# Kernel tuning notes

Measured on AMD Instinct MI355X. Metric: run time of the kernel, lower is better.

## Reference

```python
import jax, jax.numpy as jnp
import numpy as np

B, H, W = 4, 512, 512   # batch_size and spatial_shape of the SparseConvTensor
N, C = 200000, 256
K, P = 7, 3             # kernel_size, padding (submanifold: K = 2P+1)


def setup_inputs() -> dict:
    key = jax.random.key(0)
    k1, k2, k3, k4 = jax.random.split(key, 4)
    # unique active voxel coordinates via a permutation of the flat grid
    flat = jax.random.permutation(k1, B * H * W)[:N]
    b = (flat // (H * W)).astype(jnp.int32)
    y = ((flat // W) % H).astype(jnp.int32)
    x = (flat % W).astype(jnp.int32)
    indices = jnp.stack([b, y, x], axis=1)  # [N, 3] like spconv (batch, y, x)
    features = jax.random.normal(k2, (N, C), dtype=jnp.float32)
    # per-channel 7x7 depthwise kernels (spconv SubMConv2d(1,1,k) per channel)
    weight = jax.random.normal(k3, (C, K, K), dtype=jnp.float32) * (1.0 / K)
    bias = jax.random.normal(k4, (C,), dtype=jnp.float32) * 0.1
    return {"features": features, "indices": indices, "weight": weight, "bias": bias}


def reference(features, indices, weight, bias):
    """Submanifold depthwise 7x7 conv: outputs only at active sites,
    gathering only active neighbors (inactive sites contribute zero).
    Equivalent to the per-channel SubMConv2d loop, fused across channels."""
    n = features.shape[0]
    b, y, x = indices[:, 0], indices[:, 1], indices[:, 2]
    # dense map from voxel -> row index in features (-1 = inactive); this is the
    # "rulebook" built ONCE and shared by all channels
    idx_map = jnp.full((B, H, W), -1, dtype=jnp.int32)
    idx_map = idx_map.at[b, y, x].set(jnp.arange(n, dtype=jnp.int32))

    out = jnp.zeros_like(features)
    for dy in range(K):          # fixed 7x7 taps: 49-way unroll, vectorized over N, C
        for dx in range(K):
            yy = y + (dy - P)
            xx = x + (dx - P)
            inb = (yy >= 0) & (yy < H) & (xx >= 0) & (xx < W)
            nb = idx_map[b, jnp.clip(yy, 0, H - 1), jnp.clip(xx, 0, W - 1)]
            valid = inb & (nb >= 0)
            f = jnp.where(valid[:, None], features[jnp.maximum(nb, 0)], 0.0)  # [N, C]
            out = out + f * weight[None, :, dy, dx]
    return out + bias[None, :]
```

## Files before the change

### kernel.cpp

```cpp
#include <hip/hip_runtime.h>

#define BB 4
#define HH 512
#define WW 512
#define KK 7
#define PP 3
#define CC 256
#define RH 64
#define RW 32
#define SH (RH + 2 * PP)
#define SW (RW + 2 * PP)
#define NT 1024
#define NWAVE (NT / 64)
#define NREG (BB * (HH / RH) * (WW / RW))

__global__ void smconv_scatter(const int* __restrict__ idx,
                               int* __restrict__ idx_map, int n) {
    int i = blockIdx.x * blockDim.x + threadIdx.x;
    if (i >= n) return;
    int b = idx[i * 3 + 0];
    int y = idx[i * 3 + 1];
    int x = idx[i * 3 + 2];
    idx_map[((size_t)b * HH + y) * WW + x] = i;
}

__global__ void smconv_wt(const float* __restrict__ w, float* __restrict__ w_t) {
    int i = blockIdx.x * blockDim.x + threadIdx.x;
    if (i >= KK * KK * CC) return;
    int tap = i / CC;
    int c = i - tap * CC;
    w_t[i] = w[c * KK * KK + tap];
}

__global__ void __launch_bounds__(NT)
smconv_conv_region(const float* __restrict__ feat,
                   const float* __restrict__ w_t,
                   const float* __restrict__ bias,
                   const int* __restrict__ idx_map,
                   float* __restrict__ out) {
    __shared__ int smap[SH * SW];
    __shared__ unsigned short lst[RH * RW];
    __shared__ int wcnt[NWAVE];
    __shared__ float w_lds[KK * KK * CC];

    const int tid  = threadIdx.x;
    const int wave = tid >> 6;
    const int lane = tid & 63;

    const int r  = (blockIdx.x & 7) * 64 + (blockIdx.x >> 3);
    const int b  = r >> 7;
    const int rm = r & 127;
    const int rx = rm >> 3;
    const int ry = rm & 7;
    const int y0 = ry * RH;
    const int x0 = rx * RW;

    for (int i = tid; i < KK * KK * CC / 4; i += NT)
        ((float4*)w_lds)[i] = ((const float4*)w_t)[i];

    for (int i = tid; i < SH * SW; i += NT) {
        int gy = y0 + i / SW - PP;
        int gx = x0 + i % SW - PP;
        int v = -1;
        if (gy >= 0 && gy < HH && gx >= 0 && gx < WW)
            v = idx_map[((size_t)b * HH + gy) * WW + gx];
        smap[i] = v;
    }
    __syncthreads();

    int total = 0;
    for (int c = 0; c < RH * RW; c += NT) {
        int i = c + tid;
        int iy = i >> 5;
        int ix = i & (RW - 1);
        bool act = smap[(iy + PP) * SW + (ix + PP)] >= 0;
        unsigned long long bal = __ballot(act);
        if (lane == 0) wcnt[wave] = __popcll(bal);
        __syncthreads();
        int off = total;
        for (int w = 0; w < wave; ++w) off += wcnt[w];
        if (act)
            lst[off + __popcll(bal & ((1ull << lane) - 1))] = (unsigned short)i;
        int t2 = total;
        for (int w = 0; w < NWAVE; ++w) t2 += wcnt[w];
        total = t2;
        __syncthreads();
    }

    const int c4 = lane * 4;
    const int dy = lane / KK;
    const int dx = lane % KK;
    const float4 bv = *(const float4*)(bias + c4);

    for (int e = wave; e < total; e += NWAVE) {
        const int pos = lst[e];
        const int iy = pos >> 5;
        const int ix = pos & (RW - 1);

        int nb = -1;
        if (lane < KK * KK)
            nb = smap[(iy + dy) * SW + (ix + dx)];

        const int site = __shfl(nb, PP * KK + PP);
        unsigned long long mask = __ballot(nb >= 0);

        float4 acc = make_float4(0.f, 0.f, 0.f, 0.f);

        while (mask) {
            int t0 = __ffsll((long long)mask) - 1; mask &= mask - 1;
            bool h1 = mask != 0;
            int t1 = h1 ? __ffsll((long long)mask) - 1 : t0;
            if (h1) mask &= mask - 1;
            bool h2 = mask != 0;
            int t2 = h2 ? __ffsll((long long)mask) - 1 : t0;
            if (h2) mask &= mask - 1;
            bool h3 = mask != 0;
            int t3 = h3 ? __ffsll((long long)mask) - 1 : t0;
            if (h3) mask &= mask - 1;

            int n0 = __shfl(nb, t0);
            int n1 = __shfl(nb, t1);
            int n2 = __shfl(nb, t2);
            int n3 = __shfl(nb, t3);

            float4 f0 = *(const float4*)(feat + (size_t)n0 * CC + c4);
            float4 f1 = *(const float4*)(feat + (size_t)n1 * CC + c4);
            float4 f2 = *(const float4*)(feat + (size_t)n2 * CC + c4);
            float4 f3 = *(const float4*)(feat + (size_t)n3 * CC + c4);
            float4 w0 = *(const float4*)(w_lds + t0 * CC + c4);
            float4 w1 = *(const float4*)(w_lds + t1 * CC + c4);
            float4 w2 = *(const float4*)(w_lds + t2 * CC + c4);
            float4 w3 = *(const float4*)(w_lds + t3 * CC + c4);

            acc.x = fmaf(f0.x, w0.x, acc.x);
            acc.y = fmaf(f0.y, w0.y, acc.y);
            acc.z = fmaf(f0.z, w0.z, acc.z);
            acc.w = fmaf(f0.w, w0.w, acc.w);
            if (h1) {
                acc.x = fmaf(f1.x, w1.x, acc.x);
                acc.y = fmaf(f1.y, w1.y, acc.y);
                acc.z = fmaf(f1.z, w1.z, acc.z);
                acc.w = fmaf(f1.w, w1.w, acc.w);
            }
            if (h2) {
                acc.x = fmaf(f2.x, w2.x, acc.x);
                acc.y = fmaf(f2.y, w2.y, acc.y);
                acc.z = fmaf(f2.z, w2.z, acc.z);
                acc.w = fmaf(f2.w, w2.w, acc.w);
            }
            if (h3) {
                acc.x = fmaf(f3.x, w3.x, acc.x);
                acc.y = fmaf(f3.y, w3.y, acc.y);
                acc.z = fmaf(f3.z, w3.z, acc.z);
                acc.w = fmaf(f3.w, w3.w, acc.w);
            }
        }

        float4 o = make_float4(acc.x + bv.x, acc.y + bv.y,
                               acc.z + bv.z, acc.w + bv.w);
        *(float4*)(out + (size_t)site * CC + c4) = o;
    }
}

extern "C" void kernel_launch(void* const* d_in, const int* in_sizes, int n_in,
                              void* d_out, int out_size, void* d_ws, size_t ws_size,
                              hipStream_t stream) {
    const float* feat = (const float*)d_in[0];
    const int*   idx  = (const int*)d_in[1];
    const float* w    = (const float*)d_in[2];
    const float* bias = (const float*)d_in[3];
    float* out = (float*)d_out;

    const int n = in_sizes[0] / CC;

    int*   idx_map = (int*)d_ws;
    float* w_t     = (float*)((char*)d_ws + (size_t)BB * HH * WW * sizeof(int));

    hipMemsetAsync(idx_map, 0xFF, (size_t)BB * HH * WW * sizeof(int), stream);
    smconv_scatter<<<(n + 255) / 256, 256, 0, stream>>>(idx, idx_map, n);
    smconv_wt<<<(KK * KK * CC + 255) / 256, 256, 0, stream>>>(w, w_t);
    smconv_conv_region<<<NREG, NT, 0, stream>>>(feat, w_t, bias, idx_map, out);
}
```

Before: 198.6 us.

## Split channels across two blocks per region with smaller blocks and float2 lanes

Each spatial region is now handled by two 512-thread blocks, each covering 128 channels, so every wave lane processes a float2 rather than a float4. This halves the per-block weight LDS footprint and doubles the block count, aiming for higher occupancy and more concurrent gathers. Lane shuffles for uniform values are replaced with readlane. The cost is that the neighbor map and active list are built twice per region, and each gather row access becomes narrower, 512 bytes per wave.

```diff
diff --git a/kernel.cpp b/kernel.cpp
--- a/kernel.cpp
+++ b/kernel.cpp
@@ -10,9 +10,12 @@
 #define RW 32
 #define SH (RH + 2 * PP)
 #define SW (RW + 2 * PP)
-#define NT 1024
+#define NT 512
 #define NWAVE (NT / 64)
-#define NREG (BB * (HH / RH) * (WW / RW))
+#define NCHUNK 2
+#define CHF 128
+#define NREGN (BB * (HH / RH) * (WW / RW))
+#define NBLK (NREGN * NCHUNK)
 
 __global__ void smconv_scatter(const int* __restrict__ idx,
                                int* __restrict__ idx_map, int n) {
@@ -32,31 +35,36 @@
     w_t[i] = w[c * KK * KK + tap];
 }
 
-__global__ void __launch_bounds__(NT)
-smconv_conv_region(const float* __restrict__ feat,
-                   const float* __restrict__ w_t,
-                   const float* __restrict__ bias,
-                   const int* __restrict__ idx_map,
-                   float* __restrict__ out) {
+__global__ void __launch_bounds__(NT, 8)
+smconv_conv_c2(const float* __restrict__ feat,
+               const float* __restrict__ w_t,
+               const float* __restrict__ bias,
+               const int* __restrict__ idx_map,
+               float* __restrict__ out) {
     __shared__ int smap[SH * SW];
     __shared__ unsigned short lst[RH * RW];
     __shared__ int wcnt[NWAVE];
-    __shared__ float w_lds[KK * KK * CC];
+    __shared__ float w_lds[KK * KK * CHF];
 
     const int tid  = threadIdx.x;
     const int wave = tid >> 6;
     const int lane = tid & 63;
 
-    const int r  = (blockIdx.x & 7) * 64 + (blockIdx.x >> 3);
-    const int b  = r >> 7;
-    const int rm = r & 127;
+    const int Wk    = (blockIdx.x & 7) * (NBLK / 8) + (blockIdx.x >> 3);
+    const int reg   = Wk >> 1;
+    const int chunk = Wk & 1;
+    const int b  = reg >> 7;
+    const int rm = reg & 127;
     const int rx = rm >> 3;
     const int ry = rm & 7;
     const int y0 = ry * RH;
     const int x0 = rx * RW;
 
-    for (int i = tid; i < KK * KK * CC / 4; i += NT)
-        ((float4*)w_lds)[i] = ((const float4*)w_t)[i];
+    for (int i = tid; i < KK * KK * CHF / 4; i += NT) {
+        int t = i >> 5, j = i & 31;
+        ((float4*)w_lds)[i] =
+            ((const float4*)w_t)[t * (CC / 4) + chunk * (CHF / 4) + j];
+    }
 
     for (int i = tid; i < SH * SW; i += NT) {
         int gy = y0 + i / SW - PP;
@@ -69,8 +77,8 @@
     __syncthreads();
 
     int total = 0;
-    for (int c = 0; c < RH * RW; c += NT) {
-        int i = c + tid;
+    for (int c0 = 0; c0 < RH * RW; c0 += NT) {
+        int i = c0 + tid;
         int iy = i >> 5;
         int ix = i & (RW - 1);
         bool act = smap[(iy + PP) * SW + (ix + PP)] >= 0;
@@ -87,10 +95,13 @@
         __syncthreads();
     }
 
-    const int c4 = lane * 4;
     const int dy = lane / KK;
     const int dx = lane % KK;
-    const float4 bv = *(const float4*)(bias + c4);
+    const float2* feat2 = (const float2*)feat;
+    const float2* wlds2 = (const float2*)w_lds;
+    float2* out2 = (float2*)out;
+    const int co = chunk * (CHF / 2) + lane;
+    const float2 bv = ((const float2*)bias)[co];
 
     for (int e = wave; e < total; e += NWAVE) {
         const int pos = lst[e];
@@ -101,64 +112,53 @@
         if (lane < KK * KK)
             nb = smap[(iy + dy) * SW + (ix + dx)];
 
-        const int site = __shfl(nb, PP * KK + PP);
+        const int site = __builtin_amdgcn_readlane(nb, PP * KK + PP);
         unsigned long long mask = __ballot(nb >= 0);
 
-        float4 acc = make_float4(0.f, 0.f, 0.f, 0.f);
+        float2 acc = make_float2(0.f, 0.f);
 
         while (mask) {
             int t0 = __ffsll((long long)mask) - 1; mask &= mask - 1;
             bool h1 = mask != 0;
-            int t1 = h1 ? __ffsll((long long)mask) - 1 : t0;
-            if (h1) mask &= mask - 1;
+            int t1 = h1 ? __ffsll((long long)mask) - 1 : t0; if (h1) mask &= mask - 1;
             bool h2 = mask != 0;
-            int t2 = h2 ? __ffsll((long long)mask) - 1 : t0;
-            if (h2) mask &= mask - 1;
+            int t2 = h2 ? __ffsll((long long)mask) - 1 : t0; if (h2) mask &= mask - 1;
             bool h3 = mask != 0;
-            int t3 = h3 ? __ffsll((long long)mask) - 1 : t0;
-            if (h3) mask &= mask - 1;
+            int t3 = h3 ? __ffsll((long long)mask) - 1 : t0; if (h3) mask &= mask - 1;
 
-            int n0 = __shfl(nb, t0);
-            int n1 = __shfl(nb, t1);
-            int n2 = __shfl(nb, t2);
-            int n3 = __shfl(nb, t3);
+            int n0 = __builtin_amdgcn_readlane(nb, t0);
+            int n1 = __builtin_amdgcn_readlane(nb, t1);
+            int n2 = __builtin_amdgcn_readlane(nb, t2);
+            int n3 = __builtin_amdgcn_readlane(nb, t3);
 
-            float4 f0 = *(const float4*)(feat + (size_t)n0 * CC + c4);
-            float4 f1 = *(const float4*)(feat + (size_t)n1 * CC + c4);
-            float4 f2 = *(const float4*)(feat + (size_t)n2 * CC + c4);
-            float4 f3 = *(const float4*)(feat + (size_t)n3 * CC + c4);
-            float4 w0 = *(const float4*)(w_lds + t0 * CC + c4);
-            float4 w1 = *(const float4*)(w_lds + t1 * CC + c4);
-            float4 w2 = *(const float4*)(w_lds + t2 * CC + c4);
-            float4 w3 = *(const float4*)(w_lds + t3 * CC + c4);
+            float2 f0 = feat2[(size_t)n0 * (CC / 2) + co];
+            float2 f1 = feat2[(size_t)n1 * (CC / 2) + co];
+            float2 f2 = feat2[(size_t)n2 * (CC / 2) + co];
+            float2 f3 = feat2[(size_t)n3 * (CC / 2) + co];
+
+            float2 w0 = wlds2[t0 * (CHF / 2) + lane];
+            float2 w1 = wlds2[t1 * (CHF / 2) + lane];
+            float2 w2 = wlds2[t2 * (CHF / 2) + lane];
+            float2 w3 = wlds2[t3 * (CHF / 2) + lane];
 
             acc.x = fmaf(f0.x, w0.x, acc.x);
             acc.y = fmaf(f0.y, w0.y, acc.y);
-            acc.z = fmaf(f0.z, w0.z, acc.z);
-            acc.w = fmaf(f0.w, w0.w, acc.w);
             if (h1) {
                 acc.x = fmaf(f1.x, w1.x, acc.x);
                 acc.y = fmaf(f1.y, w1.y, acc.y);
-                acc.z = fmaf(f1.z, w1.z, acc.z);
-                acc.w = fmaf(f1.w, w1.w, acc.w);
             }
             if (h2) {
                 acc.x = fmaf(f2.x, w2.x, acc.x);
                 acc.y = fmaf(f2.y, w2.y, acc.y);
-                acc.z = fmaf(f2.z, w2.z, acc.z);
-                acc.w = fmaf(f2.w, w2.w, acc.w);
             }
             if (h3) {
                 acc.x = fmaf(f3.x, w3.x, acc.x);
                 acc.y = fmaf(f3.y, w3.y, acc.y);
-                acc.z = fmaf(f3.z, w3.z, acc.z);
-                acc.w = fmaf(f3.w, w3.w, acc.w);
             }
         }
 
-        float4 o = make_float4(acc.x + bv.x, acc.y + bv.y,
-                               acc.z + bv.z, acc.w + bv.w);
-        *(float4*)(out + (size_t)site * CC + c4) = o;
+        out2[(size_t)site * (CC / 2) + co] = make_float2(acc.x + bv.x,
+                                                         acc.y + bv.y);
     }
 }
 
@@ -179,5 +179,5 @@
     hipMemsetAsync(idx_map, 0xFF, (size_t)BB * HH * WW * sizeof(int), stream);
     smconv_scatter<<<(n + 255) / 256, 256, 0, stream>>>(idx, idx_map, n);
     smconv_wt<<<(KK * KK * CC + 255) / 256, 256, 0, stream>>>(w, w_t);
-    smconv_conv_region<<<NREG, NT, 0, stream>>>(feat, w_t, bias, idx_map, out);
+    smconv_conv_c2<<<NBLK, NT, 0, stream>>>(feat, w_t, bias, idx_map, out);
 }
```

After: 254.1 us. +27.9%, slower.
